# Optimization experiments

Hardware: AMD Instinct MI355X
Metric: run time of the kernel (lower is better)

## Reference

```python
import jax, jax.numpy as jnp
import numpy as np

NEG_SLOPE = 0.01  # torch F.leaky_relu default

def leaky_relu(x):
    return jnp.where(x >= 0, x, NEG_SLOPE * x)

def setup_inputs() -> dict:
    key = jax.random.key(0)
    ks = jax.random.split(key, 16)
    N, D, H, L = 2048, 512, 256, 16
    # normalized-adjacency-like matrix: row sums ~0.5 to keep activations sane
    A_hat = jax.random.uniform(ks[0], (N, N), dtype=jnp.float32) / N
    X = jax.random.normal(ks[1], (N, D), dtype=jnp.float32)
    eps = jax.random.normal(ks[2], (N, L), dtype=jnp.float32)
    def lin(k, fan_out, fan_in):
        s = 1.0 / np.sqrt(fan_in)
        kw, kb = jax.random.split(k)
        W = jax.random.uniform(kw, (fan_out, fan_in), minval=-s, maxval=s, dtype=jnp.float32)
        b = jax.random.uniform(kb, (fan_out,), minval=-s, maxval=s, dtype=jnp.float32)
        return W, b
    W1, b1 = lin(ks[3], H, D)          # gcn1
    Wmu, bmu = lin(ks[4], L, H)        # gcn2_mu
    Wlv, blv = lin(ks[5], L, H)        # gcn2_logvar
    Wd1, bd1 = lin(ks[6], 2 * L, 2 * L)  # decoder_fc1
    Wd2, bd2 = lin(ks[7], 1, 2 * L)      # decoder_fc2
    return {"A_hat": A_hat, "X": X, "eps": eps,
            "W1": W1, "b1": b1, "Wmu": Wmu, "bmu": bmu,
            "Wlv": Wlv, "blv": blv, "Wd1": Wd1, "bd1": bd1,
            "Wd2": Wd2, "bd2": bd2}

def reference(A_hat, X, eps, W1, b1, Wmu, bmu, Wlv, blv, Wd1, bd1, Wd2, bd2):
    L = Wmu.shape[0]
    # --- encode: two GCN layers (A_hat @ X) @ W.T + b ---
    Hh = leaky_relu((A_hat @ X) @ W1.T + b1)           # [N, H]
    AH = A_hat @ Hh                                    # [N, H]
    mu = AH @ Wmu.T + bmu                              # [N, L]
    logvar = AH @ Wlv.T + blv                          # [N, L]
    # --- reparameterize ---
    Z = mu + eps * jnp.exp(0.5 * logvar)               # [N, L]
    # --- decode: pairwise MLP on concat(Z_i, Z_j), vectorized ---
    # fc1(concat(Zi,Zj)) = Zi @ Wd1[:, :L].T + Zj @ Wd1[:, L:].T + bd1
    P = Z @ Wd1[:, :L].T                               # [N, 2L]
    Q = Z @ Wd1[:, L:].T                               # [N, 2L]
    h = leaky_relu(P[:, None, :] + Q[None, :, :] + bd1)  # [N, N, 2L]
    A_pred = jax.nn.sigmoid(jnp.einsum('nmh,h->nm', h, Wd2[0]) + bd2[0])  # [N, N]
    return (A_pred, mu, logvar)
```

## Files before the change

### kernel.cpp

```cpp
#include <hip/hip_runtime.h>

#define NNODE 2048
#define DD    512
#define HHID  256
#define LLAT  16
#define H2    32

typedef __attribute__((ext_vector_type(8))) short  short8;
typedef __attribute__((ext_vector_type(4))) float  f32x4;

__device__ __forceinline__ unsigned short f2bf(float x) {
    unsigned int u = __float_as_uint(x);
    unsigned int r = (u + 0x7fffu + ((u >> 16) & 1u)) >> 16;
    return (unsigned short)r;
}
__device__ __forceinline__ float bf2f(unsigned short u) {
    return __uint_as_float(((unsigned int)u) << 16);
}

__global__ __launch_bounds__(256) void t0_cvt(const float* __restrict__ A,
                                              const float* __restrict__ X,
                                              const float* __restrict__ W1,
                                              unsigned short* __restrict__ Abf,
                                              unsigned short* __restrict__ Xbf,
                                              unsigned short* __restrict__ W1bf) {
    const int NT = 1343488;
    for (int v = blockIdx.x * 256 + threadIdx.x; v < NT; v += gridDim.x * 256) {
        const float* src; unsigned short* dst; int off;
        if (v < 1048576)      { src = A;  dst = Abf;  off = v; }
        else if (v < 1310720) { src = X;  dst = Xbf;  off = v - 1048576; }
        else                  { src = W1; dst = W1bf; off = v - 1310720; }
        float4 f = ((const float4*)src)[off];
        short4 h;
        h.x = (short)f2bf(f.x); h.y = (short)f2bf(f.y);
        h.z = (short)f2bf(f.z); h.w = (short)f2bf(f.w);
        ((short4*)dst)[off] = h;
    }
}

__global__ __launch_bounds__(256) void t1_mfma(const unsigned short* __restrict__ W1bf,
                                               const unsigned short* __restrict__ Xbf,
                                               float* __restrict__ XWp) {
    __shared__ __align__(16) unsigned short Ab[64][40];
    __shared__ __align__(16) unsigned short Bb[64][40];
    const int tid = threadIdx.x;
    const int n0 = blockIdx.x * 64;
    const int h0 = blockIdx.y * 64;
    const int ks = blockIdx.z;
    const int lane = tid & 63, wave = tid >> 6;
    const int wm = wave >> 1, wn = wave & 1;
    const int lm = lane & 15, lk = (lane >> 4) * 8;
    const int sr = tid >> 2, sc = (tid & 3) * 8;
    f32x4 acc[2][2] = {};
    for (int it = 0; it < 4; ++it) {
        int kk = ks * 128 + it * 32;
        *(uint4*)&Ab[sr][sc] = *(const uint4*)(W1bf + (size_t)(h0 + sr) * DD + kk + sc);
        *(uint4*)&Bb[sr][sc] = *(const uint4*)(Xbf  + (size_t)(n0 + sr) * DD + kk + sc);
        __syncthreads();
        short8 a0 = *(const short8*)&Ab[wm * 32 + lm][lk];
        short8 a1 = *(const short8*)&Ab[wm * 32 + 16 + lm][lk];
        short8 b0 = *(const short8*)&Bb[wn * 32 + lm][lk];
        short8 b1 = *(const short8*)&Bb[wn * 32 + 16 + lm][lk];
        acc[0][0] = __builtin_amdgcn_mfma_f32_16x16x32_bf16(a0, b0, acc[0][0], 0, 0, 0);
        acc[0][1] = __builtin_amdgcn_mfma_f32_16x16x32_bf16(a0, b1, acc[0][1], 0, 0, 0);
        acc[1][0] = __builtin_amdgcn_mfma_f32_16x16x32_bf16(a1, b0, acc[1][0], 0, 0, 0);
        acc[1][1] = __builtin_amdgcn_mfma_f32_16x16x32_bf16(a1, b1, acc[1][1], 0, 0, 0);
        __syncthreads();
    }
    float* outp = XWp + (size_t)ks * 524288;
    #pragma unroll
    for (int mi = 0; mi < 2; ++mi)
        #pragma unroll
        for (int ni = 0; ni < 2; ++ni)
            #pragma unroll
            for (int r = 0; r < 4; ++r) {
                int row = h0 + wm * 32 + mi * 16 + (lane >> 4) * 4 + r;
                int col = n0 + wn * 32 + ni * 16 + lm;
                outp[(size_t)row * NNODE + col] = acc[mi][ni][r];
            }
}

__global__ __launch_bounds__(256) void t1r(const float* __restrict__ XWp,
                                           unsigned short* __restrict__ XWt) {
    int v = blockIdx.x * 256 + threadIdx.x;
    const float4* p = (const float4*)XWp;
    float4 a = p[v];
    float4 b = p[v + 131072];
    float4 c = p[v + 262144];
    float4 d = p[v + 393216];
    float4 s;
    s.x = (a.x + b.x) + (c.x + d.x);
    s.y = (a.y + b.y) + (c.y + d.y);
    s.z = (a.z + b.z) + (c.z + d.z);
    s.w = (a.w + b.w) + (c.w + d.w);
    short4 h;
    h.x = (short)f2bf(s.x); h.y = (short)f2bf(s.y);
    h.z = (short)f2bf(s.z); h.w = (short)f2bf(s.w);
    ((short4*)XWt)[v] = h;
}

__global__ __launch_bounds__(256) void t2_mfma(const unsigned short* __restrict__ Abf,
                                               const unsigned short* __restrict__ XWt,
                                               float* __restrict__ Hp) {
    __shared__ __align__(16) unsigned short Ab[64][40];
    __shared__ __align__(16) unsigned short Bb[64][40];
    const int tid = threadIdx.x;
    const int m0 = blockIdx.x * 64;
    const int n0 = blockIdx.y * 64;
    const int ks = blockIdx.z;
    const int lane = tid & 63, wave = tid >> 6;
    const int wm = wave >> 1, wn = wave & 1;
    const int lm = lane & 15, lk = (lane >> 4) * 8;
    const int sr = tid >> 2, sc = (tid & 3) * 8;
    f32x4 acc[2][2] = {};
    for (int it = 0; it < 16; ++it) {
        int kk = ks * 512 + it * 32;
        *(uint4*)&Ab[sr][sc] = *(const uint4*)(Abf + (size_t)(m0 + sr) * NNODE + kk + sc);
        *(uint4*)&Bb[sr][sc] = *(const uint4*)(XWt + (size_t)(n0 + sr) * NNODE + kk + sc);
        __syncthreads();
        short8 a0 = *(const short8*)&Ab[wm * 32 + lm][lk];
        short8 a1 = *(const short8*)&Ab[wm * 32 + 16 + lm][lk];
        short8 b0 = *(const short8*)&Bb[wn * 32 + lm][lk];
        short8 b1 = *(const short8*)&Bb[wn * 32 + 16 + lm][lk];
        acc[0][0] = __builtin_amdgcn_mfma_f32_16x16x32_bf16(a0, b0, acc[0][0], 0, 0, 0);
        acc[0][1] = __builtin_amdgcn_mfma_f32_16x16x32_bf16(a0, b1, acc[0][1], 0, 0, 0);
        acc[1][0] = __builtin_amdgcn_mfma_f32_16x16x32_bf16(a1, b0, acc[1][0], 0, 0, 0);
        acc[1][1] = __builtin_amdgcn_mfma_f32_16x16x32_bf16(a1, b1, acc[1][1], 0, 0, 0);
        __syncthreads();
    }
    float* outp = Hp + (size_t)ks * 524288;
    #pragma unroll
    for (int mi = 0; mi < 2; ++mi)
        #pragma unroll
        for (int ni = 0; ni < 2; ++ni)
            #pragma unroll
            for (int r = 0; r < 4; ++r) {
                int row = m0 + wm * 32 + mi * 16 + (lane >> 4) * 4 + r;
                int col = n0 + wn * 32 + ni * 16 + lm;
                outp[(size_t)row * HHID + col] = acc[mi][ni][r];
            }
}

__global__ __launch_bounds__(256) void t2r(const float* __restrict__ Hp,
                                           const float* __restrict__ b1,
                                           unsigned short* __restrict__ Hbf) {
    int v = blockIdx.x * 256 + threadIdx.x;
    const float4* p = (const float4*)Hp;
    float4 a = p[v];
    float4 b = p[v + 131072];
    float4 c = p[v + 262144];
    float4 d = p[v + 393216];
    int dcol = (v & 63) * 4;
    float4 bb = *(const float4*)(b1 + dcol);
    float4 s;
    s.x = (a.x + b.x) + (c.x + d.x) + bb.x;
    s.y = (a.y + b.y) + (c.y + d.y) + bb.y;
    s.z = (a.z + b.z) + (c.z + d.z) + bb.z;
    s.w = (a.w + b.w) + (c.w + d.w) + bb.w;
    s.x = fmaxf(s.x, 0.01f * s.x);
    s.y = fmaxf(s.y, 0.01f * s.y);
    s.z = fmaxf(s.z, 0.01f * s.z);
    s.w = fmaxf(s.w, 0.01f * s.w);
    short4 h;
    h.x = (short)f2bf(s.x); h.y = (short)f2bf(s.y);
    h.z = (short)f2bf(s.z); h.w = (short)f2bf(s.w);
    ((short4*)Hbf)[v] = h;
}

__global__ __launch_bounds__(256) void t3_g(const unsigned short* __restrict__ Hbf,
                                            const float* __restrict__ Wmu,
                                            const float* __restrict__ Wlv,
                                            unsigned short* __restrict__ Gt) {
    __shared__ float Hs[8][260];
    __shared__ float Ws[32][260];
    const int tid = threadIdx.x;
    const int n0 = blockIdx.x * 8;
    #pragma unroll
    for (int s = 0; s < 8; ++s) {
        int idx = tid + s * 256;
        int row = idx >> 6, c = (idx & 63) * 4;
        const float* src = (row < 16) ? (Wmu + (size_t)row * HHID)
                                      : (Wlv + (size_t)(row - 16) * HHID);
        *(float4*)&Ws[row][c] = *(const float4*)(src + c);
    }
    {
        int r = tid >> 5, seg = tid & 31;
        int d = seg * 8;
        ushort4 u0 = *(const ushort4*)(Hbf + (size_t)(n0 + r) * HHID + d);
        ushort4 u1 = *(const ushort4*)(Hbf + (size_t)(n0 + r) * HHID + d + 4);
        Hs[r][d + 0] = bf2f(u0.x); Hs[r][d + 1] = bf2f(u0.y);
        Hs[r][d + 2] = bf2f(u0.z); Hs[r][d + 3] = bf2f(u0.w);
        Hs[r][d + 4] = bf2f(u1.x); Hs[r][d + 5] = bf2f(u1.y);
        Hs[r][d + 6] = bf2f(u1.z); Hs[r][d + 7] = bf2f(u1.w);
    }
    __syncthreads();
    const int r = tid >> 5, j = tid & 31;
    float acc = 0.f;
    #pragma unroll 8
    for (int d4 = 0; d4 < 64; ++d4) {
        float4 a = *(const float4*)&Hs[r][d4 * 4];
        float4 b = *(const float4*)&Ws[j][d4 * 4];
        acc += a.x * b.x + a.y * b.y + a.z * b.z + a.w * b.w;
    }
    Gt[(size_t)j * NNODE + n0 + r] = f2bf(acc);
}

__global__ __launch_bounds__(256) void t4_mfma(const unsigned short* __restrict__ Abf,
                                               const unsigned short* __restrict__ Gt,
                                               float* __restrict__ Mp) {
    __shared__ __align__(16) unsigned short Ab[64][40];
    __shared__ __align__(16) unsigned short Bb[32][40];
    const int tid = threadIdx.x;
    const int m0 = blockIdx.x * 64;
    const int ks = blockIdx.y;
    const int lane = tid & 63, wave = tid >> 6;
    const int lm = lane & 15, lk = (lane >> 4) * 8;
    const int sr = tid >> 2, sc = (tid & 3) * 8;
    f32x4 acc[2] = {};
    for (int it = 0; it < 8; ++it) {
        int kk = ks * 256 + it * 32;
        *(uint4*)&Ab[sr][sc] = *(const uint4*)(Abf + (size_t)(m0 + sr) * NNODE + kk + sc);
        if (tid < 128) {
            int row = tid >> 2, c = (tid & 3) * 8;
            *(uint4*)&Bb[row][c] = *(const uint4*)(Gt + (size_t)row * NNODE + kk + c);
        }
        __syncthreads();
        short8 a  = *(const short8*)&Ab[wave * 16 + lm][lk];
        short8 b0 = *(const short8*)&Bb[lm][lk];
        short8 b1 = *(const short8*)&Bb[16 + lm][lk];
        acc[0] = __builtin_amdgcn_mfma_f32_16x16x32_bf16(a, b0, acc[0], 0, 0, 0);
        acc[1] = __builtin_amdgcn_mfma_f32_16x16x32_bf16(a, b1, acc[1], 0, 0, 0);
        __syncthreads();
    }
    float* outp = Mp + (size_t)ks * 65536;
    #pragma unroll
    for (int ni = 0; ni < 2; ++ni)
        #pragma unroll
        for (int r = 0; r < 4; ++r) {
            int row = m0 + wave * 16 + (lane >> 4) * 4 + r;
            int col = ni * 16 + lm;
            outp[(size_t)row * H2 + col] = acc[ni][r];
        }
}

__global__ __launch_bounds__(256) void t5_z(const float* __restrict__ Mp,
                                            const float* __restrict__ bmu,
                                            const float* __restrict__ blv,
                                            const float* __restrict__ eps,
                                            const float* __restrict__ Wd1,
                                            const float* __restrict__ bd1,
                                            const float* __restrict__ Wd2,
                                            float* __restrict__ out_mu,
                                            float* __restrict__ out_lv,
                                            float* __restrict__ Pp,
                                            float* __restrict__ Qq,
                                            float* __restrict__ WP,
                                            float* __restrict__ WQ) {
    __shared__ float Zs[16][16];
    __shared__ float Psh[16][32];
    __shared__ float Qsh[16][32];
    const int tid = threadIdx.x;
    const int n0 = blockIdx.x * 16;
    {
        int nl = tid >> 4, l = tid & 15;
        int n = n0 + nl;
        float m = bmu[l], lv = blv[l];
        #pragma unroll
        for (int s = 0; s < 8; ++s) {
            m  += Mp[(size_t)s * 65536 + (size_t)n * H2 + l];
            lv += Mp[(size_t)s * 65536 + (size_t)n * H2 + 16 + l];
        }
        out_mu[(size_t)n * LLAT + l] = m;
        out_lv[(size_t)n * LLAT + l] = lv;
        Zs[nl][l] = m + eps[(size_t)n * LLAT + l] * __expf(0.5f * lv);
    }
    __syncthreads();
    #pragma unroll
    for (int p = 0; p < 2; ++p) {
        int idx = tid + p * 256;
        int nl = idx >> 5, o = idx & 31;
        int n = n0 + nl;
        float ap = bd1[o], aq = 0.f;
        #pragma unroll
        for (int l = 0; l < 16; ++l) {
            float z = Zs[nl][l];
            ap = fmaf(z, Wd1[o * H2 + l],      ap);
            aq = fmaf(z, Wd1[o * H2 + 16 + l], aq);
        }
        Pp[(size_t)n * H2 + o] = ap;
        Qq[(size_t)n * H2 + o] = aq;
        Psh[nl][o] = ap;
        Qsh[nl][o] = aq;
    }
    __syncthreads();
    if (tid < 32) {
        int nl = tid & 15, sel = tid >> 4;
        float a = 0.f;
        if (sel == 0) {
            #pragma unroll
            for (int o = 0; o < 32; ++o) a = fmaf(Wd2[o], Psh[nl][o], a);
            WP[n0 + nl] = a;
        } else {
            #pragma unroll
            for (int o = 0; o < 32; ++o) a = fmaf(Wd2[o], Qsh[nl][o], a);
            WQ[n0 + nl] = a;
        }
    }
}

__global__ __launch_bounds__(256) void t6_dec(const float* __restrict__ Pp,
                                              const float* __restrict__ Qq,
                                              const float* __restrict__ WP,
                                              const float* __restrict__ WQ,
                                              const float* __restrict__ Wd2,
                                              const float* __restrict__ bd2,
                                              float* __restrict__ Apred) {
    __shared__ float Qt[32][68];
    __shared__ float Ws2[32];
    __shared__ float WQs[64];
    const int tid = threadIdx.x;
    const int j0 = blockIdx.x * 64, i0 = blockIdx.y * 16;
    #pragma unroll
    for (int s = 0; s < 8; ++s) {
        int idx = tid + s * 256;
        int j = idx >> 5, o = idx & 31;
        Qt[o][j] = Qq[(size_t)(j0 + j) * H2 + o];
    }
    if (tid < 32) Ws2[tid] = Wd2[tid];
    if (tid >= 64 && tid < 128) WQs[tid - 64] = WQ[j0 + tid - 64];
    const int i = i0 + (tid >> 4);
    const int jq = tid & 15;
    float p[32];
    const float4* P4 = (const float4*)(Pp + (size_t)i * H2);
    #pragma unroll
    for (int c = 0; c < 8; ++c) {
        float4 v = P4[c];
        p[c * 4] = v.x; p[c * 4 + 1] = v.y; p[c * 4 + 2] = v.z; p[c * 4 + 3] = v.w;
    }
    const float WPi = WP[i];
    __syncthreads();
    f32x4 acc = {0.f, 0.f, 0.f, 0.f};
    #pragma unroll
    for (int o = 0; o < 32; ++o) {
        float4 q = *(const float4*)&Qt[o][jq * 4];
        float w = Ws2[o], po = p[o];
        acc[0] = fmaf(w, fabsf(po + q.x), acc[0]);
        acc[1] = fmaf(w, fabsf(po + q.y), acc[1]);
        acc[2] = fmaf(w, fabsf(po + q.z), acc[2]);
        acc[3] = fmaf(w, fabsf(po + q.w), acc[3]);
    }
    float4 wq = *(const float4*)&WQs[jq * 4];
    const float base = fmaf(0.505f, WPi, bd2[0]);
    float4 r;
    float l0 = fmaf(0.505f, wq.x, fmaf(0.495f, acc[0], base));
    float l1 = fmaf(0.505f, wq.y, fmaf(0.495f, acc[1], base));
    float l2 = fmaf(0.505f, wq.z, fmaf(0.495f, acc[2], base));
    float l3 = fmaf(0.505f, wq.w, fmaf(0.495f, acc[3], base));
    r.x = 1.f / (1.f + __expf(-l0));
    r.y = 1.f / (1.f + __expf(-l1));
    r.z = 1.f / (1.f + __expf(-l2));
    r.w = 1.f / (1.f + __expf(-l3));
    *(float4*)(Apred + (size_t)i * NNODE + j0 + jq * 4) = r;
}

extern "C" void kernel_launch(void* const* d_in, const int* in_sizes, int n_in,
                              void* d_out, int out_size, void* d_ws, size_t ws_size,
                              hipStream_t stream) {
    const float* A   = (const float*)d_in[0];
    const float* X   = (const float*)d_in[1];
    const float* eps = (const float*)d_in[2];
    const float* W1  = (const float*)d_in[3];
    const float* b1  = (const float*)d_in[4];
    const float* Wmu = (const float*)d_in[5];
    const float* bmu = (const float*)d_in[6];
    const float* Wlv = (const float*)d_in[7];
    const float* blv = (const float*)d_in[8];
    const float* Wd1 = (const float*)d_in[9];
    const float* bd1 = (const float*)d_in[10];
    const float* Wd2 = (const float*)d_in[11];
    const float* bd2 = (const float*)d_in[12];
    float* out = (float*)d_out;
    char* ws = (char*)d_ws;

    unsigned short* Abf  = (unsigned short*)(ws);
    unsigned short* Xbf  = (unsigned short*)(ws + 8388608);
    unsigned short* W1bf = (unsigned short*)(ws + 10485760);
    float*          XWp  = (float*)(ws + 10747904);
    unsigned short* XWt  = (unsigned short*)(ws + 19136512);
    float*          Hp   = (float*)(ws + 20185088);
    unsigned short* Hbf  = (unsigned short*)(ws + 28573696);
    unsigned short* Gt   = (unsigned short*)(ws + 29622272);
    float*          Mp   = (float*)(ws + 29753344);
    float*          Pp   = (float*)(ws + 31850496);
    float*          Qq   = (float*)(ws + 32112640);
    float*          WP   = (float*)(ws + 32374784);
    float*          WQ   = (float*)(ws + 32382976);

    float* out_mu = out + (size_t)NNODE * NNODE;
    float* out_lv = out_mu + NNODE * LLAT;

    t0_cvt <<<2048,            256, 0, stream>>>(A, X, W1, Abf, Xbf, W1bf);
    t1_mfma<<<dim3(32, 4, 4),  256, 0, stream>>>(W1bf, Xbf, XWp);
    t1r    <<<512,             256, 0, stream>>>(XWp, XWt);
    t2_mfma<<<dim3(32, 4, 4),  256, 0, stream>>>(Abf, XWt, Hp);
    t2r    <<<512,             256, 0, stream>>>(Hp, b1, Hbf);
    t3_g   <<<256,             256, 0, stream>>>(Hbf, Wmu, Wlv, Gt);
    t4_mfma<<<dim3(32, 8),     256, 0, stream>>>(Abf, Gt, Mp);
    t5_z   <<<128,             256, 0, stream>>>(Mp, bmu, blv, eps, Wd1, bd1, Wd2,
                                                 out_mu, out_lv, Pp, Qq, WP, WQ);
    t6_dec <<<dim3(32, 128),   256, 0, stream>>>(Pp, Qq, WP, WQ, Wd2, bd2, out);
}
```

Before: 141.5 us.

## Fuse conversion and split-K reductions into neighbouring GEMM kernels

Removes the standalone conversion kernel and both split-K reduction kernels, cutting the launch count from nine to six. The first GEMM now converts X and W1 to bf16 on load, converts A_hat in the same kernel, and writes its partial sums as bf16. The second GEMM sums those partials while staging tiles, and the G kernel reduces the H partials and applies bias and leaky ReLU itself. Costs: each K-slice of k2 re-reads and re-sums the four partial buffers, and rounding the partials to bf16 before summing adds some precision loss.

Result: no change. 142.5 us (+0.7%).

```diff
diff --git a/kernel.cpp b/kernel.cpp
--- a/kernel.cpp
+++ b/kernel.cpp
@@ -17,33 +17,48 @@
 __device__ __forceinline__ float bf2f(unsigned short u) {
     return __uint_as_float(((unsigned int)u) << 16);
 }
-
-__global__ __launch_bounds__(256) void t0_cvt(const float* __restrict__ A,
-                                              const float* __restrict__ X,
-                                              const float* __restrict__ W1,
-                                              unsigned short* __restrict__ Abf,
-                                              unsigned short* __restrict__ Xbf,
-                                              unsigned short* __restrict__ W1bf) {
-    const int NT = 1343488;
-    for (int v = blockIdx.x * 256 + threadIdx.x; v < NT; v += gridDim.x * 256) {
-        const float* src; unsigned short* dst; int off;
-        if (v < 1048576)      { src = A;  dst = Abf;  off = v; }
-        else if (v < 1310720) { src = X;  dst = Xbf;  off = v - 1048576; }
-        else                  { src = W1; dst = W1bf; off = v - 1310720; }
-        float4 f = ((const float4*)src)[off];
+__device__ __forceinline__ uint4 cvt8u(const float* p) {
+    float4 f0 = *(const float4*)p;
+    float4 f1 = *(const float4*)(p + 4);
+    uint4 r;
+    unsigned short* s = (unsigned short*)&r;
+    s[0] = f2bf(f0.x); s[1] = f2bf(f0.y); s[2] = f2bf(f0.z); s[3] = f2bf(f0.w);
+    s[4] = f2bf(f1.x); s[5] = f2bf(f1.y); s[6] = f2bf(f1.z); s[7] = f2bf(f1.w);
+    return r;
+}
+__device__ __forceinline__ uint4 sum4bf(const unsigned short* base, size_t off) {
+    uint4 a = *(const uint4*)(base + off);
+    uint4 b = *(const uint4*)(base + off + 524288);
+    uint4 c = *(const uint4*)(base + off + 1048576);
+    uint4 d = *(const uint4*)(base + off + 1572864);
+    const unsigned short* pa = (const unsigned short*)&a;
+    const unsigned short* pb = (const unsigned short*)&b;
+    const unsigned short* pc = (const unsigned short*)&c;
+    const unsigned short* pd = (const unsigned short*)&d;
+    uint4 r;
+    unsigned short* pr = (unsigned short*)&r;
+    #pragma unroll
+    for (int e = 0; e < 8; ++e)
+        pr[e] = f2bf((bf2f(pa[e]) + bf2f(pb[e])) + (bf2f(pc[e]) + bf2f(pd[e])));
+    return r;
+}
+
+__global__ __launch_bounds__(256) void k1_xw(const float* __restrict__ A,
+                                             const float* __restrict__ X,
+                                             const float* __restrict__ W1,
+                                             unsigned short* __restrict__ Abf,
+                                             unsigned short* __restrict__ XWpb) {
+    __shared__ __align__(16) unsigned short Ab[64][40];
+    __shared__ __align__(16) unsigned short Bb[64][40];
+    const int tid = threadIdx.x;
+    const int bid = blockIdx.x + blockIdx.y * 32 + blockIdx.z * 128;
+    for (int v = bid * 256 + tid; v < 1048576; v += 131072) {
+        float4 f = ((const float4*)A)[v];
         short4 h;
         h.x = (short)f2bf(f.x); h.y = (short)f2bf(f.y);
         h.z = (short)f2bf(f.z); h.w = (short)f2bf(f.w);
-        ((short4*)dst)[off] = h;
-    }
-}
-
-__global__ __launch_bounds__(256) void t1_mfma(const unsigned short* __restrict__ W1bf,
-                                               const unsigned short* __restrict__ Xbf,
-                                               float* __restrict__ XWp) {
-    __shared__ __align__(16) unsigned short Ab[64][40];
-    __shared__ __align__(16) unsigned short Bb[64][40];
-    const int tid = threadIdx.x;
+        ((short4*)Abf)[v] = h;
+    }
     const int n0 = blockIdx.x * 64;
     const int h0 = blockIdx.y * 64;
     const int ks = blockIdx.z;
@@ -54,8 +69,8 @@
     f32x4 acc[2][2] = {};
     for (int it = 0; it < 4; ++it) {
         int kk = ks * 128 + it * 32;
-        *(uint4*)&Ab[sr][sc] = *(const uint4*)(W1bf + (size_t)(h0 + sr) * DD + kk + sc);
-        *(uint4*)&Bb[sr][sc] = *(const uint4*)(Xbf  + (size_t)(n0 + sr) * DD + kk + sc);
+        *(uint4*)&Ab[sr][sc] = cvt8u(W1 + (size_t)(h0 + sr) * DD + kk + sc);
+        *(uint4*)&Bb[sr][sc] = cvt8u(X  + (size_t)(n0 + sr) * DD + kk + sc);
         __syncthreads();
         short8 a0 = *(const short8*)&Ab[wm * 32 + lm][lk];
         short8 a1 = *(const short8*)&Ab[wm * 32 + 16 + lm][lk];
@@ -67,7 +82,7 @@
         acc[1][1] = __builtin_amdgcn_mfma_f32_16x16x32_bf16(a1, b1, acc[1][1], 0, 0, 0);
         __syncthreads();
     }
-    float* outp = XWp + (size_t)ks * 524288;
+    unsigned short* outp = XWpb + (size_t)ks * 524288;
     #pragma unroll
     for (int mi = 0; mi < 2; ++mi)
         #pragma unroll
@@ -76,32 +91,13 @@
             for (int r = 0; r < 4; ++r) {
                 int row = h0 + wm * 32 + mi * 16 + (lane >> 4) * 4 + r;
                 int col = n0 + wn * 32 + ni * 16 + lm;
-                outp[(size_t)row * NNODE + col] = acc[mi][ni][r];
+                outp[(size_t)row * NNODE + col] = f2bf(acc[mi][ni][r]);
             }
 }
 
-__global__ __launch_bounds__(256) void t1r(const float* __restrict__ XWp,
-                                           unsigned short* __restrict__ XWt) {
-    int v = blockIdx.x * 256 + threadIdx.x;
-    const float4* p = (const float4*)XWp;
-    float4 a = p[v];
-    float4 b = p[v + 131072];
-    float4 c = p[v + 262144];
-    float4 d = p[v + 393216];
-    float4 s;
-    s.x = (a.x + b.x) + (c.x + d.x);
-    s.y = (a.y + b.y) + (c.y + d.y);
-    s.z = (a.z + b.z) + (c.z + d.z);
-    s.w = (a.w + b.w) + (c.w + d.w);
-    short4 h;
-    h.x = (short)f2bf(s.x); h.y = (short)f2bf(s.y);
-    h.z = (short)f2bf(s.z); h.w = (short)f2bf(s.w);
-    ((short4*)XWt)[v] = h;
-}
-
-__global__ __launch_bounds__(256) void t2_mfma(const unsigned short* __restrict__ Abf,
-                                               const unsigned short* __restrict__ XWt,
-                                               float* __restrict__ Hp) {
+__global__ __launch_bounds__(256) void k2_h(const unsigned short* __restrict__ Abf,
+                                            const unsigned short* __restrict__ XWpb,
+                                            float* __restrict__ Hp) {
     __shared__ __align__(16) unsigned short Ab[64][40];
     __shared__ __align__(16) unsigned short Bb[64][40];
     const int tid = threadIdx.x;
@@ -116,7 +112,7 @@
     for (int it = 0; it < 16; ++it) {
         int kk = ks * 512 + it * 32;
         *(uint4*)&Ab[sr][sc] = *(const uint4*)(Abf + (size_t)(m0 + sr) * NNODE + kk + sc);
-        *(uint4*)&Bb[sr][sc] = *(const uint4*)(XWt + (size_t)(n0 + sr) * NNODE + kk + sc);
+        *(uint4*)&Bb[sr][sc] = sum4bf(XWpb, (size_t)(n0 + sr) * NNODE + kk + sc);
         __syncthreads();
         short8 a0 = *(const short8*)&Ab[wm * 32 + lm][lk];
         short8 a1 = *(const short8*)&Ab[wm * 32 + 16 + lm][lk];
@@ -141,33 +137,8 @@
             }
 }
 
-__global__ __launch_bounds__(256) void t2r(const float* __restrict__ Hp,
-                                           const float* __restrict__ b1,
-                                           unsigned short* __restrict__ Hbf) {
-    int v = blockIdx.x * 256 + threadIdx.x;
-    const float4* p = (const float4*)Hp;
-    float4 a = p[v];
-    float4 b = p[v + 131072];
-    float4 c = p[v + 262144];
-    float4 d = p[v + 393216];
-    int dcol = (v & 63) * 4;
-    float4 bb = *(const float4*)(b1 + dcol);
-    float4 s;
-    s.x = (a.x + b.x) + (c.x + d.x) + bb.x;
-    s.y = (a.y + b.y) + (c.y + d.y) + bb.y;
-    s.z = (a.z + b.z) + (c.z + d.z) + bb.z;
-    s.w = (a.w + b.w) + (c.w + d.w) + bb.w;
-    s.x = fmaxf(s.x, 0.01f * s.x);
-    s.y = fmaxf(s.y, 0.01f * s.y);
-    s.z = fmaxf(s.z, 0.01f * s.z);
-    s.w = fmaxf(s.w, 0.01f * s.w);
-    short4 h;
-    h.x = (short)f2bf(s.x); h.y = (short)f2bf(s.y);
-    h.z = (short)f2bf(s.z); h.w = (short)f2bf(s.w);
-    ((short4*)Hbf)[v] = h;
-}
-
-__global__ __launch_bounds__(256) void t3_g(const unsigned short* __restrict__ Hbf,
+__global__ __launch_bounds__(256) void k3_g(const float* __restrict__ Hp,
+                                            const float* __restrict__ b1,
                                             const float* __restrict__ Wmu,
                                             const float* __restrict__ Wlv,
                                             unsigned short* __restrict__ Gt) {
@@ -186,12 +157,25 @@
     {
         int r = tid >> 5, seg = tid & 31;
         int d = seg * 8;
-        ushort4 u0 = *(const ushort4*)(Hbf + (size_t)(n0 + r) * HHID + d);
-        ushort4 u1 = *(const ushort4*)(Hbf + (size_t)(n0 + r) * HHID + d + 4);
-        Hs[r][d + 0] = bf2f(u0.x); Hs[r][d + 1] = bf2f(u0.y);
-        Hs[r][d + 2] = bf2f(u0.z); Hs[r][d + 3] = bf2f(u0.w);
-        Hs[r][d + 4] = bf2f(u1.x); Hs[r][d + 5] = bf2f(u1.y);
-        Hs[r][d + 6] = bf2f(u1.z); Hs[r][d + 7] = bf2f(u1.w);
+        size_t off = (size_t)(n0 + r) * HHID + d;
+        #pragma unroll
+        for (int t = 0; t < 2; ++t) {
+            float4 s0 = *(const float4*)(Hp + off + t * 4);
+            float4 s1 = *(const float4*)(Hp + off + 524288 + t * 4);
+            float4 s2 = *(const float4*)(Hp + off + 1048576 + t * 4);
+            float4 s3 = *(const float4*)(Hp + off + 1572864 + t * 4);
+            float4 bb = *(const float4*)(b1 + d + t * 4);
+            float4 o;
+            o.x = (s0.x + s1.x) + (s2.x + s3.x) + bb.x;
+            o.y = (s0.y + s1.y) + (s2.y + s3.y) + bb.y;
+            o.z = (s0.z + s1.z) + (s2.z + s3.z) + bb.z;
+            o.w = (s0.w + s1.w) + (s2.w + s3.w) + bb.w;
+            o.x = fmaxf(o.x, 0.01f * o.x);
+            o.y = fmaxf(o.y, 0.01f * o.y);
+            o.z = fmaxf(o.z, 0.01f * o.z);
+            o.w = fmaxf(o.w, 0.01f * o.w);
+            *(float4*)&Hs[r][d + t * 4] = o;
+        }
     }
     __syncthreads();
     const int r = tid >> 5, j = tid & 31;
@@ -205,9 +189,9 @@
     Gt[(size_t)j * NNODE + n0 + r] = f2bf(acc);
 }
 
-__global__ __launch_bounds__(256) void t4_mfma(const unsigned short* __restrict__ Abf,
-                                               const unsigned short* __restrict__ Gt,
-                                               float* __restrict__ Mp) {
+__global__ __launch_bounds__(256) void k4_m(const unsigned short* __restrict__ Abf,
+                                            const unsigned short* __restrict__ Gt,
+                                            float* __restrict__ Mp) {
     __shared__ __align__(16) unsigned short Ab[64][40];
     __shared__ __align__(16) unsigned short Bb[32][40];
     const int tid = threadIdx.x;
@@ -243,7 +227,7 @@
         }
 }
 
-__global__ __launch_bounds__(256) void t5_z(const float* __restrict__ Mp,
+__global__ __launch_bounds__(256) void k5_z(const float* __restrict__ Mp,
                                             const float* __restrict__ bmu,
                                             const float* __restrict__ blv,
                                             const float* __restrict__ eps,
@@ -308,7 +292,7 @@
     }
 }
 
-__global__ __launch_bounds__(256) void t6_dec(const float* __restrict__ Pp,
+__global__ __launch_bounds__(256) void k6_dec(const float* __restrict__ Pp,
                                               const float* __restrict__ Qq,
                                               const float* __restrict__ WP,
                                               const float* __restrict__ WQ,
@@ -383,30 +367,23 @@
     char* ws = (char*)d_ws;
 
     unsigned short* Abf  = (unsigned short*)(ws);
-    unsigned short* Xbf  = (unsigned short*)(ws + 8388608);
-    unsigned short* W1bf = (unsigned short*)(ws + 10485760);
-    float*          XWp  = (float*)(ws + 10747904);
-    unsigned short* XWt  = (unsigned short*)(ws + 19136512);
-    float*          Hp   = (float*)(ws + 20185088);
-    unsigned short* Hbf  = (unsigned short*)(ws + 28573696);
-    unsigned short* Gt   = (unsigned short*)(ws + 29622272);
-    float*          Mp   = (float*)(ws + 29753344);
-    float*          Pp   = (float*)(ws + 31850496);
-    float*          Qq   = (float*)(ws + 32112640);
-    float*          WP   = (float*)(ws + 32374784);
-    float*          WQ   = (float*)(ws + 32382976);
+    unsigned short* XWpb = (unsigned short*)(ws + 8388608);
+    float*          Hp   = (float*)(ws + 12582912);
+    unsigned short* Gt   = (unsigned short*)(ws + 20971520);
+    float*          Mp   = (float*)(ws + 21102592);
+    float*          Pp   = (float*)(ws + 23199744);
+    float*          Qq   = (float*)(ws + 23461888);
+    float*          WP   = (float*)(ws + 23724032);
+    float*          WQ   = (float*)(ws + 23732224);
 
     float* out_mu = out + (size_t)NNODE * NNODE;
     float* out_lv = out_mu + NNODE * LLAT;
 
-    t0_cvt <<<2048,            256, 0, stream>>>(A, X, W1, Abf, Xbf, W1bf);
-    t1_mfma<<<dim3(32, 4, 4),  256, 0, stream>>>(W1bf, Xbf, XWp);
-    t1r    <<<512,             256, 0, stream>>>(XWp, XWt);
-    t2_mfma<<<dim3(32, 4, 4),  256, 0, stream>>>(Abf, XWt, Hp);
-    t2r    <<<512,             256, 0, stream>>>(Hp, b1, Hbf);
-    t3_g   <<<256,             256, 0, stream>>>(Hbf, Wmu, Wlv, Gt);
-    t4_mfma<<<dim3(32, 8),     256, 0, stream>>>(Abf, Gt, Mp);
-    t5_z   <<<128,             256, 0, stream>>>(Mp, bmu, blv, eps, Wd1, bd1, Wd2,
-                                                 out_mu, out_lv, Pp, Qq, WP, WQ);
-    t6_dec <<<dim3(32, 128),   256, 0, stream>>>(Pp, Qq, WP, WQ, Wd2, bd2, out);
-}
+    k1_xw <<<dim3(32, 4, 4), 256, 0, stream>>>(A, X, W1, Abf, XWpb);
+    k2_h  <<<dim3(32, 4, 4), 256, 0, stream>>>(Abf, XWpb, Hp);
+    k3_g  <<<256,            256, 0, stream>>>(Hp, b1, Wmu, Wlv, Gt);
+    k4_m  <<<dim3(32, 8),    256, 0, stream>>>(Abf, Gt, Mp);
+    k5_z  <<<128,            256, 0, stream>>>(Mp, bmu, blv, eps, Wd1, bd1, Wd2,
+                                               out_mu, out_lv, Pp, Qq, WP, WQ);
+    k6_dec<<<dim3(32, 128),  256, 0, stream>>>(Pp, Qq, WP, WQ, Wd2, bd2, out);
+}
```
